# Optimization experiments

Hardware: AMD Instinct MI355X
Metric: run time of the kernel (lower is better)

The kernel has to match this reference:

```python
import jax, jax.numpy as jnp
import numpy as np


def setup_inputs() -> dict:
    key = jax.random.key(0)
    k1, k2 = jax.random.split(key, 2)
    N, HrWr, HW = 16, 4096, 1024
    num_levels, max_k = 3, 5
    return {
        "R_combined": jax.random.normal(k1, (N, HrWr, HW), dtype=jnp.float32),
        "k_logits": jax.random.normal(k2, (num_levels, max_k), dtype=jnp.float32),
        "temperature": jnp.array(1.0, dtype=jnp.float32),
        "max_k": 5,
        "num_levels": 3,
    }


def reference(R_combined, k_logits, temperature, max_k, num_levels):
    # --- gumbel-softmax over k choices (soft samples, as in F.gumbel_softmax) ---
    gkey = jax.random.key(42)
    u = jax.random.uniform(gkey, k_logits.shape, k_logits.dtype,
                           minval=1e-6, maxval=1.0 - 1e-6)
    gumbels = -jnp.log(-jnp.log(u))
    k_probs = jax.nn.softmax((k_logits + gumbels) / temperature, axis=-1)  # [L, max_k]
    k_hard = jnp.argmax(k_probs, axis=-1) + 1                              # [L] ints in [1, max_k]
    k_soft = jnp.sum(k_probs * jnp.arange(1, max_k + 1, dtype=k_probs.dtype), axis=-1)
    # straight-through estimator
    k_selected = (jax.lax.stop_gradient(k_hard.astype(k_soft.dtype))
                  + k_soft - jax.lax.stop_gradient(k_soft))

    # --- top-k over HrWr axis (dim=1); take max_k once, then per-level mask.
    # topk(k) + pad to max_k with (-inf, 0)  ==  topk(max_k) masked at rank >= k,
    # since top_k returns sorted-descending values (matches torch.topk sorted=True).
    x = jnp.swapaxes(R_combined, 1, 2)           # [N, HW, HrWr]
    vals, idx = jax.lax.top_k(x, max_k)          # [N, HW, max_k]
    vals = jnp.swapaxes(vals, 1, 2)              # [N, max_k, HW]
    idx = jnp.swapaxes(idx, 1, 2)                # [N, max_k, HW]

    rank = jnp.arange(max_k)                     # [max_k]
    mask = (rank[None, :] < k_hard[:, None])[:, None, :, None]  # [L, 1, max_k, 1]
    R_star_levels = jnp.where(mask, vals[None], -jnp.inf)       # [L, N, max_k, HW]
    R_idx_levels = jnp.where(mask, idx[None], 0)                # [L, N, max_k, HW]

    return (k_selected, R_star_levels, R_idx_levels)
```

## Files before the change

kernel.cpp:

```cpp
#include <hip/hip_runtime.h>
#include <math.h>
#include <float.h>
#include <stdint.h>

#define N_N   16
#define HRWR  4096
#define HW_   1024
#define LVLS  3
#define MAXK  5
#define SEGS  8
#define SEGLEN (HRWR / SEGS)
#define COLS  32

#define NEG_SENTINEL (-1.0e30f)

__device__ __forceinline__ unsigned rotl32(unsigned x, unsigned r) {
  return (x << r) | (x >> (32u - r));
}

__device__ __forceinline__ bool beats(float v, int i, float V, int I) {
  return (v > V) || (v == V && i < I);
}

__global__ __launch_bounds__(256)
void dynk_kernel(const float* __restrict__ R,
                 const float* __restrict__ k_logits,
                 const float* __restrict__ temperature,
                 float* __restrict__ out)
{
  __shared__ float    s_vals[SEGS][COLS][MAXK];
  __shared__ int      s_idx [SEGS][COLS][MAXK];
  __shared__ unsigned s_bits[LVLS * MAXK];
  __shared__ int      s_khard[LVLS];

  const int tid = threadIdx.x;
  const int c   = tid & (COLS - 1);
  const int s   = tid >> 5;
  const int b   = blockIdx.x;
  const int n   = b >> 5;
  const int hw  = ((b & 31) << 5) | c;

  if (tid < LVLS * MAXK) {
    unsigned x0 = 0u, x1 = (unsigned)tid;
    const unsigned k0 = 0u, k1 = 42u;
    const unsigned k2 = k0 ^ k1 ^ 0x1BD11BDAu;
    x0 += k0; x1 += k1;
#define TF_RND(rot) { x0 += x1; x1 = rotl32(x1, rot); x1 ^= x0; }
    TF_RND(13) TF_RND(15) TF_RND(26) TF_RND(6)  x0 += k1; x1 += k2 + 1u;
    TF_RND(17) TF_RND(29) TF_RND(16) TF_RND(24) x0 += k2; x1 += k0 + 2u;
    TF_RND(13) TF_RND(15) TF_RND(26) TF_RND(6)  x0 += k0; x1 += k1 + 3u;
    TF_RND(17) TF_RND(29) TF_RND(16) TF_RND(24) x0 += k1; x1 += k2 + 4u;
    TF_RND(13) TF_RND(15) TF_RND(26) TF_RND(6)  x0 += k2; x1 += k0 + 5u;
#undef TF_RND
    s_bits[tid] = x0 ^ x1;
  }
  __syncthreads();

  if (tid == 0) {
    const float T = temperature[0];
    for (int l = 0; l < LVLS; ++l) {
      float z[MAXK], p[MAXK];
      float zmax = -INFINITY;
      for (int k = 0; k < MAXK; ++k) {
        unsigned bits = s_bits[l * MAXK + k];
        float f = __uint_as_float((bits >> 9) | 0x3f800000u) - 1.0f;
        const float mn = 1e-6f;
        const float mx = 1.0f - 1e-6f;
        float u = fmaxf(mn, f * (mx - mn) + mn);
        float g = -logf(-logf(u));
        z[k] = (k_logits[l * MAXK + k] + g) / T;
        zmax = fmaxf(zmax, z[k]);
      }
      float sum = 0.0f;
      for (int k = 0; k < MAXK; ++k) { p[k] = expf(z[k] - zmax); sum += p[k]; }
      float pmax = -INFINITY; int arg = 0; float ksoft = 0.0f;
      for (int k = 0; k < MAXK; ++k) {
        p[k] = p[k] / sum;
        if (p[k] > pmax) { pmax = p[k]; arg = k; }
        ksoft += p[k] * (float)(k + 1);
      }
      const int khard = arg + 1;
      s_khard[l] = khard;
      if (b == 0) out[l] = ((float)khard + ksoft) - ksoft;
    }
  }

  float tv[MAXK];
  int   ti[MAXK];
#pragma unroll
  for (int k = 0; k < MAXK; ++k) { tv[k] = -INFINITY; ti[k] = 0x7fffffff; }

  const float* __restrict__ base =
      R + ((size_t)n * HRWR + (size_t)s * SEGLEN) * HW_ + hw;
  const int r0 = s * SEGLEN;

  for (int r = 0; r < SEGLEN; r += 8) {
    float v[8];
#pragma unroll
    for (int j = 0; j < 8; ++j) v[j] = base[(size_t)(r + j) * HW_];
#pragma unroll
    for (int j = 0; j < 8; ++j) {
      const float val = v[j];
      if (val > tv[MAXK - 1]) {
        tv[MAXK - 1] = val;
        ti[MAXK - 1] = r0 + r + j;
#pragma unroll
        for (int k = MAXK - 1; k > 0; --k) {
          if (tv[k] > tv[k - 1]) {
            float tf = tv[k]; tv[k] = tv[k - 1]; tv[k - 1] = tf;
            int   tt = ti[k]; ti[k] = ti[k - 1]; ti[k - 1] = tt;
          }
        }
      }
    }
  }

#pragma unroll
  for (int k = 0; k < MAXK; ++k) { s_vals[s][c][k] = tv[k]; s_idx[s][c][k] = ti[k]; }
  __syncthreads();

  if (tid < COLS) {
    const int cc = tid;
    float fv[MAXK]; int fi[MAXK];
#pragma unroll
    for (int k = 0; k < MAXK; ++k) { fv[k] = s_vals[0][cc][k]; fi[k] = s_idx[0][cc][k]; }
    for (int ss = 1; ss < SEGS; ++ss) {
#pragma unroll
      for (int k = 0; k < MAXK; ++k) {
        const float v = s_vals[ss][cc][k];
        const int   i = s_idx [ss][cc][k];
        if (beats(v, i, fv[MAXK - 1], fi[MAXK - 1])) {
          fv[MAXK - 1] = v; fi[MAXK - 1] = i;
#pragma unroll
          for (int k2 = MAXK - 1; k2 > 0; --k2) {
            if (beats(fv[k2], fi[k2], fv[k2 - 1], fi[k2 - 1])) {
              float tf = fv[k2]; fv[k2] = fv[k2 - 1]; fv[k2 - 1] = tf;
              int   tt = fi[k2]; fi[k2] = fi[k2 - 1]; fi[k2 - 1] = tt;
            }
          }
        }
      }
    }

    const int hww = ((b & 31) << 5) | cc;
    float* __restrict__ star = out + LVLS;
    float* __restrict__ idxo = out + LVLS + (size_t)LVLS * N_N * MAXK * HW_;
#pragma unroll
    for (int l = 0; l < LVLS; ++l) {
      const int kh = s_khard[l];
#pragma unroll
      for (int k = 0; k < MAXK; ++k) {
        const bool on = (k < kh);
        const size_t off = (((size_t)l * N_N + n) * MAXK + k) * HW_ + hww;
        star[off] = on ? fv[k] : NEG_SENTINEL;
        idxo[off] = on ? (float)fi[k] : 0.0f;
      }
    }
  }
}

extern "C" void kernel_launch(void* const* d_in, const int* in_sizes, int n_in,
                              void* d_out, int out_size, void* d_ws, size_t ws_size,
                              hipStream_t stream) {
  const float* R    = (const float*)d_in[0];
  const float* kl   = (const float*)d_in[1];
  const float* temp = (const float*)d_in[2];
  float* out = (float*)d_out;

  dynk_kernel<<<dim3(512), dim3(256), 0, stream>>>(R, kl, temp, out);
}
```

Measured before the change: 410.4 us.

## Split top-k into float4 partial-scan kernel and separate merge kernel

Replaces the single kernel with two. The first has each thread scan 4 adjacent columns using float4 loads with double-buffered register prefetch, over 16 row chunks per batch item, and writes per-chunk top-5 lists to workspace. The second kernel merges the 16 partial lists per column and writes the masked outputs. The aim is wider, better-pipelined loads to get closer to HBM bandwidth when streaming the 256MB input. The cost is higher register pressure from four top-k lists per thread, only 256 blocks in the scan kernel, and an extra launch plus a workspace round trip.

```diff
diff --git a/kernel.cpp b/kernel.cpp
--- a/kernel.cpp
+++ b/kernel.cpp
@@ -8,9 +8,9 @@
 #define HW_   1024
 #define LVLS  3
 #define MAXK  5
-#define SEGS  8
-#define SEGLEN (HRWR / SEGS)
-#define COLS  32
+#define RC    16
+#define RCLEN (HRWR / RC)
+#define BATCH 8
 
 #define NEG_SENTINEL (-1.0e30f)
 
@@ -22,23 +22,98 @@
   return (v > V) || (v == V && i < I);
 }
 
+__device__ __forceinline__ void proc_one(float v, int idx,
+                                         float (&tv)[MAXK], int (&ti)[MAXK]) {
+  if (v > tv[MAXK - 1]) {
+    tv[MAXK - 1] = v;
+    ti[MAXK - 1] = idx;
+#pragma unroll
+    for (int k = MAXK - 1; k > 0; --k) {
+      if (tv[k] > tv[k - 1]) {
+        float tf = tv[k]; tv[k] = tv[k - 1]; tv[k - 1] = tf;
+        int   tt = ti[k]; ti[k] = ti[k - 1]; ti[k - 1] = tt;
+      }
+    }
+  }
+}
+
 __global__ __launch_bounds__(256)
-void dynk_kernel(const float* __restrict__ R,
-                 const float* __restrict__ k_logits,
-                 const float* __restrict__ temperature,
-                 float* __restrict__ out)
+void partial_topk(const float* __restrict__ R,
+                  float* __restrict__ ws_val,
+                  int*   __restrict__ ws_idx)
 {
-  __shared__ float    s_vals[SEGS][COLS][MAXK];
-  __shared__ int      s_idx [SEGS][COLS][MAXK];
+  const int tid  = threadIdx.x;
+  const int b    = blockIdx.x;
+  const int n    = b >> 4;
+  const int rc   = b & 15;
+  const int col0 = tid << 2;
+
+  float tv[4][MAXK];
+  int   ti[4][MAXK];
+#pragma unroll
+  for (int cc = 0; cc < 4; ++cc)
+#pragma unroll
+    for (int k = 0; k < MAXK; ++k) { tv[cc][k] = -INFINITY; ti[cc][k] = 0x7fffffff; }
+
+  const float* __restrict__ base =
+      R + ((size_t)n * HRWR + (size_t)rc * RCLEN) * HW_ + col0;
+  const int r0 = rc * RCLEN;
+
+  float4 bufA[BATCH], bufB[BATCH];
+
+#pragma unroll
+  for (int j = 0; j < BATCH; ++j)
+    bufA[j] = *(const float4*)(base + (size_t)j * HW_);
+
+  for (int t = 0; t < RCLEN; t += 2 * BATCH) {
+#pragma unroll
+    for (int j = 0; j < BATCH; ++j)
+      bufB[j] = *(const float4*)(base + (size_t)(t + BATCH + j) * HW_);
+#pragma unroll
+    for (int j = 0; j < BATCH; ++j) {
+      const int ridx = r0 + t + j;
+      proc_one(bufA[j].x, ridx, tv[0], ti[0]);
+      proc_one(bufA[j].y, ridx, tv[1], ti[1]);
+      proc_one(bufA[j].z, ridx, tv[2], ti[2]);
+      proc_one(bufA[j].w, ridx, tv[3], ti[3]);
+    }
+    if (t + 2 * BATCH < RCLEN) {
+#pragma unroll
+      for (int j = 0; j < BATCH; ++j)
+        bufA[j] = *(const float4*)(base + (size_t)(t + 2 * BATCH + j) * HW_);
+    }
+#pragma unroll
+    for (int j = 0; j < BATCH; ++j) {
+      const int ridx = r0 + t + BATCH + j;
+      proc_one(bufB[j].x, ridx, tv[0], ti[0]);
+      proc_one(bufB[j].y, ridx, tv[1], ti[1]);
+      proc_one(bufB[j].z, ridx, tv[2], ti[2]);
+      proc_one(bufB[j].w, ridx, tv[3], ti[3]);
+    }
+  }
+
+  float* __restrict__ wv = ws_val + (((size_t)n * HW_ + col0) * RC + rc) * MAXK;
+  int*   __restrict__ wi = ws_idx + (((size_t)n * HW_ + col0) * RC + rc) * MAXK;
+#pragma unroll
+  for (int cc = 0; cc < 4; ++cc)
+#pragma unroll
+    for (int k = 0; k < MAXK; ++k) {
+      wv[(size_t)cc * RC * MAXK + k] = tv[cc][k];
+      wi[(size_t)cc * RC * MAXK + k] = ti[cc][k];
+    }
+}
+
+__global__ __launch_bounds__(256)
+void merge_topk(const float* __restrict__ ws_val,
+                const int*   __restrict__ ws_idx,
+                const float* __restrict__ k_logits,
+                const float* __restrict__ temperature,
+                float* __restrict__ out)
+{
   __shared__ unsigned s_bits[LVLS * MAXK];
   __shared__ int      s_khard[LVLS];
 
   const int tid = threadIdx.x;
-  const int c   = tid & (COLS - 1);
-  const int s   = tid >> 5;
-  const int b   = blockIdx.x;
-  const int n   = b >> 5;
-  const int hw  = ((b & 31) << 5) | c;
 
   if (tid < LVLS * MAXK) {
     unsigned x0 = 0u, x1 = (unsigned)tid;
@@ -81,80 +156,51 @@
       }
       const int khard = arg + 1;
       s_khard[l] = khard;
-      if (b == 0) out[l] = ((float)khard + ksoft) - ksoft;
-    }
-  }
-
-  float tv[MAXK];
-  int   ti[MAXK];
-#pragma unroll
-  for (int k = 0; k < MAXK; ++k) { tv[k] = -INFINITY; ti[k] = 0x7fffffff; }
-
-  const float* __restrict__ base =
-      R + ((size_t)n * HRWR + (size_t)s * SEGLEN) * HW_ + hw;
-  const int r0 = s * SEGLEN;
-
-  for (int r = 0; r < SEGLEN; r += 8) {
-    float v[8];
-#pragma unroll
-    for (int j = 0; j < 8; ++j) v[j] = base[(size_t)(r + j) * HW_];
-#pragma unroll
-    for (int j = 0; j < 8; ++j) {
-      const float val = v[j];
-      if (val > tv[MAXK - 1]) {
-        tv[MAXK - 1] = val;
-        ti[MAXK - 1] = r0 + r + j;
-#pragma unroll
-        for (int k = MAXK - 1; k > 0; --k) {
-          if (tv[k] > tv[k - 1]) {
-            float tf = tv[k]; tv[k] = tv[k - 1]; tv[k - 1] = tf;
-            int   tt = ti[k]; ti[k] = ti[k - 1]; ti[k - 1] = tt;
+      if (blockIdx.x == 0) out[l] = ((float)khard + ksoft) - ksoft;
+    }
+  }
+  __syncthreads();
+
+  const int g   = blockIdx.x * 256 + tid;
+  const int n   = g >> 10;
+  const int col = g & (HW_ - 1);
+
+  const float* __restrict__ wv = ws_val + (size_t)g * (RC * MAXK);
+  const int*   __restrict__ wi = ws_idx + (size_t)g * (RC * MAXK);
+
+  float fv[MAXK]; int fi[MAXK];
+#pragma unroll
+  for (int k = 0; k < MAXK; ++k) { fv[k] = wv[k]; fi[k] = wi[k]; }
+
+  for (int rc = 1; rc < RC; ++rc) {
+#pragma unroll
+    for (int k = 0; k < MAXK; ++k) {
+      const float v = wv[rc * MAXK + k];
+      const int   i = wi[rc * MAXK + k];
+      if (beats(v, i, fv[MAXK - 1], fi[MAXK - 1])) {
+        fv[MAXK - 1] = v; fi[MAXK - 1] = i;
+#pragma unroll
+        for (int k2 = MAXK - 1; k2 > 0; --k2) {
+          if (beats(fv[k2], fi[k2], fv[k2 - 1], fi[k2 - 1])) {
+            float tf = fv[k2]; fv[k2] = fv[k2 - 1]; fv[k2 - 1] = tf;
+            int   tt = fi[k2]; fi[k2] = fi[k2 - 1]; fi[k2 - 1] = tt;
           }
         }
       }
     }
   }
 
-#pragma unroll
-  for (int k = 0; k < MAXK; ++k) { s_vals[s][c][k] = tv[k]; s_idx[s][c][k] = ti[k]; }
-  __syncthreads();
-
-  if (tid < COLS) {
-    const int cc = tid;
-    float fv[MAXK]; int fi[MAXK];
-#pragma unroll
-    for (int k = 0; k < MAXK; ++k) { fv[k] = s_vals[0][cc][k]; fi[k] = s_idx[0][cc][k]; }
-    for (int ss = 1; ss < SEGS; ++ss) {
-#pragma unroll
-      for (int k = 0; k < MAXK; ++k) {
-        const float v = s_vals[ss][cc][k];
-        const int   i = s_idx [ss][cc][k];
-        if (beats(v, i, fv[MAXK - 1], fi[MAXK - 1])) {
-          fv[MAXK - 1] = v; fi[MAXK - 1] = i;
-#pragma unroll
-          for (int k2 = MAXK - 1; k2 > 0; --k2) {
-            if (beats(fv[k2], fi[k2], fv[k2 - 1], fi[k2 - 1])) {
-              float tf = fv[k2]; fv[k2] = fv[k2 - 1]; fv[k2 - 1] = tf;
-              int   tt = fi[k2]; fi[k2] = fi[k2 - 1]; fi[k2 - 1] = tt;
-            }
-          }
-        }
-      }
-    }
-
-    const int hww = ((b & 31) << 5) | cc;
-    float* __restrict__ star = out + LVLS;
-    float* __restrict__ idxo = out + LVLS + (size_t)LVLS * N_N * MAXK * HW_;
-#pragma unroll
-    for (int l = 0; l < LVLS; ++l) {
-      const int kh = s_khard[l];
-#pragma unroll
-      for (int k = 0; k < MAXK; ++k) {
-        const bool on = (k < kh);
-        const size_t off = (((size_t)l * N_N + n) * MAXK + k) * HW_ + hww;
-        star[off] = on ? fv[k] : NEG_SENTINEL;
-        idxo[off] = on ? (float)fi[k] : 0.0f;
-      }
+  float* __restrict__ star = out + LVLS;
+  float* __restrict__ idxo = out + LVLS + (size_t)LVLS * N_N * MAXK * HW_;
+#pragma unroll
+  for (int l = 0; l < LVLS; ++l) {
+    const int kh = s_khard[l];
+#pragma unroll
+    for (int k = 0; k < MAXK; ++k) {
+      const bool on = (k < kh);
+      const size_t off = (((size_t)l * N_N + n) * MAXK + k) * HW_ + col;
+      star[off] = on ? fv[k] : NEG_SENTINEL;
+      idxo[off] = on ? (float)fi[k] : 0.0f;
     }
   }
 }
@@ -167,5 +213,9 @@
   const float* temp = (const float*)d_in[2];
   float* out = (float*)d_out;
 
-  dynk_kernel<<<dim3(512), dim3(256), 0, stream>>>(R, kl, temp, out);
-}
+  float* ws_val = (float*)d_ws;
+  int*   ws_idx = (int*)((char*)d_ws + (size_t)N_N * HW_ * RC * MAXK * sizeof(float));
+
+  partial_topk<<<dim3(N_N * RC), dim3(256), 0, stream>>>(R, ws_val, ws_idx);
+  merge_topk<<<dim3(64), dim3(256), 0, stream>>>(ws_val, ws_idx, kl, temp, out);
+}
```

Result: slower. 419.2 us (+2.1%).
